# Performance work log

Measured on AMD Instinct MI355X. Metric: run time of the kernel, lower is better.

## Reference

```python
import jax, jax.numpy as jnp
import numpy as np

B, S, I, H, O = 256, 512, 128, 256, 1


def setup_inputs() -> dict:
    key = jax.random.key(0)
    ks = jax.random.split(key, 12)
    s_a = 1.0 / np.sqrt(H + I)
    s_g = 1.0 / np.sqrt(H)
    s_f = 1.0 / np.sqrt(H)
    return {
        "x": jax.random.normal(ks[0], (B, S, I), dtype=jnp.float32),
        # input attention linear: (H+I) -> I
        "W_a": jax.random.uniform(ks[1], (I, H + I), minval=-s_a, maxval=s_a),
        "b_a": jax.random.uniform(ks[2], (I,), minval=-s_a, maxval=s_a),
        # GRUCell params (torch layout: [3H, I] / [3H, H], gate order r,z,n)
        "W_ih": jax.random.uniform(ks[3], (3 * H, I), minval=-s_g, maxval=s_g),
        "b_ih": jax.random.uniform(ks[4], (3 * H,), minval=-s_g, maxval=s_g),
        "W_hh": jax.random.uniform(ks[5], (3 * H, H), minval=-s_g, maxval=s_g),
        "b_hh": jax.random.uniform(ks[6], (3 * H,), minval=-s_g, maxval=s_g),
        # temporal attention linear: H -> 1
        "W_t": jax.random.uniform(ks[7], (1, H), minval=-s_f, maxval=s_f),
        "b_t": jax.random.uniform(ks[8], (1,), minval=-s_f, maxval=s_f),
        # output fc: H -> O
        "W_f": jax.random.uniform(ks[9], (O, H), minval=-s_f, maxval=s_f),
        "b_f": jax.random.uniform(ks[10], (O,), minval=-s_f, maxval=s_f),
    }


def reference(x, W_a, b_a, W_ih, b_ih, W_hh, b_hh, W_t, b_t, W_f, b_f):
    def step(h, x_t):  # h: [B,H], x_t: [B,I]
        combined = jnp.concatenate([x_t, h], axis=1)            # [B, I+H]
        scores = jnp.tanh(combined @ W_a.T + b_a)               # [B, I]
        alpha = jax.nn.softmax(scores, axis=1)                  # [B, I]
        xw = alpha * x_t                                        # [B, I]
        gi = xw @ W_ih.T + b_ih                                 # [B, 3H]
        gh = h @ W_hh.T + b_hh                                  # [B, 3H]
        i_r, i_z, i_n = jnp.split(gi, 3, axis=1)
        h_r, h_z, h_n = jnp.split(gh, 3, axis=1)
        r = jax.nn.sigmoid(i_r + h_r)
        z = jax.nn.sigmoid(i_z + h_z)
        n = jnp.tanh(i_n + r * h_n)
        h_new = (1.0 - z) * n + z * h
        return h_new, h_new

    h0 = jnp.zeros((x.shape[0], W_hh.shape[1]), dtype=x.dtype)
    xs = jnp.transpose(x, (1, 0, 2))                            # [S,B,I]
    _, hs = jax.lax.scan(step, h0, xs)                          # hs: [S,B,H]
    enc = jnp.transpose(hs, (1, 0, 2))                          # [B,S,H]

    t_scores = jnp.tanh(enc @ W_t.T + b_t)                      # [B,S,1]
    beta = jax.nn.softmax(t_scores, axis=1)                     # softmax over time
    context = jnp.sum(beta * enc, axis=1)                       # [B,H]
    logits = context @ W_f.T + b_f                              # [B,O]
    return jax.nn.sigmoid(logits)
```

## Files before the change

### kernel.cpp

```cpp
#include <hip/hip_runtime.h>
#include <math.h>

#define BB 256
#define SS 512
#define II 128
#define HH 256

typedef unsigned short ushort_t;
typedef unsigned int uint32;

#define OFF_WA   0
#define OFF_BA   49152
#define OFF_WIH  49280
#define OFF_BIH  147584
#define OFF_WHH  148352
#define OFF_BHH  344960
#define OFF_WT   345728
#define OFF_BT   345984
#define OFF_WF   345992
#define OFF_BF   346248
#define OFF_WAH  346256
#define OFF_GIX  379024

#define WHH_LC   12

__device__ __forceinline__ float b2f(ushort_t u) {
    union { uint32 i; float f; } v; v.i = ((uint32)u) << 16; return v.f;
}
__device__ __forceinline__ float lo2f(uint32 w) {
    union { uint32 i; float f; } v; v.i = w << 16; return v.f;
}
__device__ __forceinline__ float hi2f(uint32 w) {
    union { uint32 i; float f; } v; v.i = w & 0xFFFF0000u; return v.f;
}
__device__ __forceinline__ ushort_t f2b(float f) {
    union { float f; uint32 i; } v; v.f = f;
    uint32 r = (v.i + 0x7FFFu + ((v.i >> 16) & 1u)) >> 16;
    return (ushort_t)r;
}
__device__ __forceinline__ uint32 pack2(float a, float b) {
    return (uint32)f2b(a) | ((uint32)f2b(b) << 16);
}

#if __has_builtin(__builtin_amdgcn_fdot2_f32_bf16)
typedef __bf16 v2bf __attribute__((ext_vector_type(2)));
__device__ __forceinline__ float dot2u(uint32 w, uint32 v, float acc) {
    return __builtin_amdgcn_fdot2_f32_bf16(
        __builtin_bit_cast(v2bf, w), __builtin_bit_cast(v2bf, v), acc, false);
}
#else
__device__ __forceinline__ float dot2u(uint32 w, uint32 v, float acc) {
    acc = fmaf(lo2f(w), lo2f(v), acc);
    return fmaf(hi2f(w), hi2f(v), acc);
}
#endif
__device__ __forceinline__ float dot4(uint4 w, uint4 v, float acc) {
    acc = dot2u(w.x, v.x, acc); acc = dot2u(w.y, v.y, acc);
    acc = dot2u(w.z, v.z, acc); return dot2u(w.w, v.w, acc);
}

__global__ void cvt_f32_bf16(const float* __restrict__ src, ushort_t* __restrict__ dst, int n) {
    int i = blockIdx.x * 256 + threadIdx.x;
    if (i < n) dst[i] = f2b(src[i]);
}

__global__ void cvt_swz(const float* __restrict__ src, ushort_t* __restrict__ dst,
                        int rows, int chunks, int srcStride, int colOff) {
    int t = blockIdx.x * 256 + threadIdx.x;
    if (t >= rows * chunks) return;
    int row = t / chunks, c = t % chunks;
    const float* s = src + (size_t)row * srcStride + colOff + c * 8;
    uint4 v;
    v.x = pack2(s[0], s[1]); v.y = pack2(s[2], s[3]);
    v.z = pack2(s[4], s[5]); v.w = pack2(s[6], s[7]);
    ((uint4*)dst)[((size_t)(row >> 6) * chunks + c) * 64 + (row & 63)] = v;
}

__global__ __launch_bounds__(512, 2) void gix_kernel(
    const float* __restrict__ x, const ushort_t* __restrict__ wsb,
    float* __restrict__ gix)
{
    const int b = blockIdx.x, tid = threadIdx.x;
    const int r4 = tid >> 7, i = tid & 127;
    __shared__ __align__(16) uint32 sxp[4][64];

    uint4 w[16];
    const uint4* wa_g = (const uint4*)(wsb + OFF_WA);
    const size_t gb = (size_t)(i >> 6) * 48 * 64 + (i & 63);
    #pragma unroll
    for (int c = 0; c < 16; ++c) w[c] = wa_g[gb + (size_t)c * 64];

    const float* xb = x + (size_t)b * SS * II;
    float* gout = gix + (size_t)b * SS * II;
    for (int j = 0; j < SS; j += 4) {
        float v = xb[(j + r4) * II + i];
        float vn = __shfl_down(v, 1);
        if (!(i & 1)) sxp[r4][i >> 1] = pack2(v, vn);
        __syncthreads();
        const uint4* sx4 = (const uint4*)sxp[r4];
        float acc = 0.f;
        #pragma unroll
        for (int c = 0; c < 16; ++c) acc = dot4(w[c], sx4[c], acc);
        gout[(j + r4) * II + i] = acc;
        __syncthreads();
    }
}

template <int GIX>
__global__ __launch_bounds__(1024, 4) void da_rnn_kernel(
    const float* __restrict__ x,
    const ushort_t* __restrict__ wsb,
    const float* __restrict__ gix,
    float* __restrict__ out)
{
    const int b    = blockIdx.x;
    const int tid  = threadIdx.x;
    const int lane = tid & 63;
    const int wv   = tid >> 6;
    const bool is_gate = (tid < 3 * HH);

    __shared__ __align__(16) uint32 whh_lds[WHH_LC * 768 * 4];
    __shared__ __align__(16) uint32 s_xh_p[192];
    __shared__ __align__(16) uint32 sxw_p[64];
    __shared__ __align__(16) float  sred[256];
    __shared__ __align__(16) float  sgi[3 * HH];
    __shared__ __align__(16) float  sgh[3 * HH];
    __shared__ __align__(16) float  sx[2][II];
    __shared__ __align__(16) float  sgix[2][II];
    __shared__ float swave[4];
    __shared__ int   flag_red;
    __shared__ int   flag_xw;

    if (tid == 0) { flag_red = 0; flag_xw = 0; }
    if (tid < II) s_xh_p[64 + tid] = 0u;

    uint4 wreg[16];
    const int a   = tid - 3 * HH;
    const int row = a & 127;
    const int s   = a >> 7;
    const uint4* whh_base = (const uint4*)(wsb + OFF_WHH) + (size_t)wv * 32 * 64 + lane;
    const uint4* wa_st = nullptr;
    float bias_i = 0.f, bias_h = 0.f, ba_a = 0.f, ba_b = 0.f;

    if (is_gate) {
        const uint4* wih_g = (const uint4*)(wsb + OFF_WIH) + (size_t)wv * 16 * 64 + lane;
        #pragma unroll
        for (int c = 0; c < 16; ++c) wreg[c] = wih_g[c * 64];
        bias_i = b2f(wsb[OFF_BIH + tid]);
        bias_h = b2f(wsb[OFF_BHH + tid]);
        #pragma unroll
        for (int c = 0; c < WHH_LC; ++c)
            ((uint4*)whh_lds)[(wv * WHH_LC + c) * 64 + lane] = whh_base[c * 64];
    } else {
        if (GIX) {
            const uint4* wah_g = (const uint4*)(wsb + OFF_WAH);
            const size_t gbh = ((size_t)(row >> 6) * 32 + s * 16) * 64 + (row & 63);
            #pragma unroll
            for (int i = 0; i < 16; ++i) wreg[i] = wah_g[gbh + (size_t)i * 64];
        } else {
            const uint4* wa_g = (const uint4*)(wsb + OFF_WA);
            const size_t gbase = ((size_t)(row >> 6) * 48 + s * 24) * 64 + (row & 63);
            #pragma unroll
            for (int i = 0; i < 16; ++i) wreg[i] = wa_g[gbase + (size_t)i * 64];
            wa_st = wa_g + gbase + (size_t)16 * 64;
        }
        ba_a = b2f(wsb[OFF_BA + lane]);
        ba_b = b2f(wsb[OFF_BA + 64 + lane]);
    }

    float h_reg = 0.f, c_reg = 0.f, m_run = -2.0f, l_run = 0.f;
    float wt_j = 0.f, wf_j = 0.f, bt_r = 0.f;
    if (tid < HH) {
        wt_j = b2f(wsb[OFF_WT + tid]);
        wf_j = b2f(wsb[OFF_WF + tid]);
        bt_r = b2f(wsb[OFF_BT]);
    }

    const float* xrow  = x + (size_t)b * SS * II;
    const float* grow0 = GIX ? (gix + (size_t)b * SS * II) : nullptr;
    if (!is_gate && a >= 64 && a < 192) {
        const int idx = a - 64;
        float v = xrow[idx];
        sx[0][idx] = v;
        if (!GIX) {
            float vn = __shfl_down(v, 1);
            if (!(idx & 1)) s_xh_p[idx >> 1] = pack2(v, vn);
        }
    }
    if (GIX && !is_gate && a >= 192) {
        const int l = a - 192;
        sgix[0][l]      = grow0[l];
        sgix[0][64 + l] = grow0[64 + l];
    }
    __syncthreads();

    const uint4* st4 = (const uint4*)s_xh_p;
    const uint4* shp = (const uint4*)s_xh_p + 16;
    const uint4* xwp = (const uint4*)sxw_p;
    const uint4* whl = (const uint4*)whh_lds + (size_t)(wv * WHH_LC) * 64 + lane;

    for (int t = 0; t < SS; ++t) {
        const int p = t & 1;

        if (is_gate) {
            float gh = bias_h;
            #pragma unroll
            for (int c = 0; c < WHH_LC; ++c) gh = dot4(whl[c * 64], shp[c], gh);
            #pragma unroll 4
            for (int c = WHH_LC; c < 32; ++c) gh = dot4(whh_base[c * 64], shp[c], gh);
            sgh[tid] = gh;
            while (__hip_atomic_load(&flag_xw, __ATOMIC_ACQUIRE,
                                     __HIP_MEMORY_SCOPE_WORKGROUP) <= t) {}
            float gi = bias_i;
            #pragma unroll
            for (int c = 0; c < 16; ++c) gi = dot4(wreg[c], xwp[c], gi);
            sgi[tid] = gi;
        } else {
            float acc = 0.f;
            if (GIX) {
                #pragma unroll
                for (int i = 0; i < 16; ++i) acc = dot4(wreg[i], shp[s * 16 + i], acc);
            } else {
                #pragma unroll
                for (int i = 0; i < 16; ++i) acc = dot4(wreg[i], st4[s * 24 + i], acc);
                #pragma unroll 4
                for (int i = 0; i < 8; ++i) acc = dot4(wa_st[i * 64], st4[s * 24 + 16 + i], acc);
            }
            sred[a] = acc;
            if (lane == 0)
                __hip_atomic_fetch_add(&flag_red, 1, __ATOMIC_ACQ_REL,
                                       __HIP_MEMORY_SCOPE_WORKGROUP);
            const int tgt = 4 * (t + 1);
            while (__hip_atomic_load(&flag_red, __ATOMIC_ACQUIRE,
                                     __HIP_MEMORY_SCOPE_WORKGROUP) < tgt) {}
            if (a < 64) {
                float s_a = sred[lane] + sred[128 + lane] + ba_a;
                float s_b = sred[64 + lane] + sred[192 + lane] + ba_b;
                if (GIX) { s_a += sgix[p][lane]; s_b += sgix[p][64 + lane]; }
                s_a = tanhf(s_a); s_b = tanhf(s_b);
                float m = fmaxf(s_a, s_b);
                for (int off = 32; off; off >>= 1) m = fmaxf(m, __shfl_xor(m, off));
                float e_a = expf(s_a - m), e_b = expf(s_b - m);
                float sum = e_a + e_b;
                for (int off = 32; off; off >>= 1) sum += __shfl_xor(sum, off);
                float inv = 1.f / sum;
                float xa = e_a * inv * sx[p][lane];
                float xb = e_b * inv * sx[p][64 + lane];
                float xa1 = __shfl_down(xa, 1), xb1 = __shfl_down(xb, 1);
                if (!(lane & 1)) {
                    sxw_p[lane >> 1]        = pack2(xa, xa1);
                    sxw_p[32 + (lane >> 1)] = pack2(xb, xb1);
                }
                if (lane == 0)
                    __hip_atomic_store(&flag_xw, t + 1, __ATOMIC_RELEASE,
                                       __HIP_MEMORY_SCOPE_WORKGROUP);
            } else if (a >= 64 && a < 192 && t + 1 < SS) {
                const int idx = a - 64;
                float v = xrow[(t + 1) * II + idx];
                sx[p ^ 1][idx] = v;
                if (!GIX) {
                    float vn = __shfl_down(v, 1);
                    if (!(idx & 1)) s_xh_p[idx >> 1] = pack2(v, vn);
                }
            } else if (GIX && a >= 192 && t + 1 < SS) {
                const float* gr = grow0 + (size_t)(t + 1) * II;
                const int l = a - 192;
                sgix[p ^ 1][l]      = gr[l];
                sgix[p ^ 1][64 + l] = gr[64 + l];
            }
        }
        __syncthreads();

        if (tid < HH) {
            const float r = 1.f / (1.f + expf(-(sgi[tid] + sgh[tid])));
            const float z = 1.f / (1.f + expf(-(sgi[tid + HH] + sgh[tid + HH])));
            const float n = tanhf(sgi[tid + 2 * HH] + r * sgh[tid + 2 * HH]);
            h_reg = (1.f - z) * n + z * h_reg;
            float hn2 = __shfl_down(h_reg, 1);
            if (!(tid & 1)) s_xh_p[64 + (tid >> 1)] = pack2(h_reg, hn2);
            float pd = wt_j * h_reg;
            for (int off = 32; off; off >>= 1) pd += __shfl_down(pd, off);
            if (lane == 0) swave[wv] = pd;
        }
        __syncthreads();

        if (tid < HH) {
            float dot = swave[0] + swave[1] + swave[2] + swave[3] + bt_r;
            float st = tanhf(dot);
            float mn = fmaxf(m_run, st);
            float aa = expf(m_run - mn), ww = expf(st - mn);
            l_run = l_run * aa + ww;
            m_run = mn;
            c_reg = c_reg * aa + ww * h_reg;
        }
    }

    __syncthreads();
    if (tid < HH) {
        float ctx = c_reg / l_run;
        float pd = wf_j * ctx;
        for (int off = 32; off; off >>= 1) pd += __shfl_down(pd, off);
        if (lane == 0) swave[wv] = pd;
    }
    __syncthreads();
    if (tid == 0) {
        float logit = swave[0] + swave[1] + swave[2] + swave[3] + b2f(wsb[OFF_BF]);
        out[b] = 1.f / (1.f + expf(-logit));
    }
}

extern "C" void kernel_launch(void* const* d_in, const int* in_sizes, int n_in,
                              void* d_out, int out_size, void* d_ws, size_t ws_size,
                              hipStream_t stream) {
    ushort_t* wsb = (ushort_t*)d_ws;
    const size_t WS_NEED = (size_t)OFF_GIX * 2 + (size_t)BB * SS * II * 4;
    const bool use_gix = ws_size >= WS_NEED;

    cvt_swz<<<dim3((128 * 48 + 255) / 256), dim3(256), 0, stream>>>(
        (const float*)d_in[1], wsb + OFF_WA, 128, 48, 384, 0);
    cvt_swz<<<dim3((768 * 16 + 255) / 256), dim3(256), 0, stream>>>(
        (const float*)d_in[3], wsb + OFF_WIH, 768, 16, 128, 0);
    cvt_swz<<<dim3((768 * 32 + 255) / 256), dim3(256), 0, stream>>>(
        (const float*)d_in[5], wsb + OFF_WHH, 768, 32, 256, 0);
    if (use_gix)
        cvt_swz<<<dim3((128 * 32 + 255) / 256), dim3(256), 0, stream>>>(
            (const float*)d_in[1], wsb + OFF_WAH, 128, 32, 384, 128);

    struct { int src_idx; int off; int n; } cv[7] = {
        {2, OFF_BA,  II}, {4, OFF_BIH, 3 * HH}, {6, OFF_BHH, 3 * HH},
        {7, OFF_WT,  HH}, {8, OFF_BT, 1}, {9, OFF_WF, HH}, {10, OFF_BF, 1},
    };
    for (int i = 0; i < 7; ++i) {
        int blocks = (cv[i].n + 255) / 256;
        cvt_f32_bf16<<<dim3(blocks), dim3(256), 0, stream>>>(
            (const float*)d_in[cv[i].src_idx], wsb + cv[i].off, cv[i].n);
    }

    float* gixf = (float*)(wsb + OFF_GIX);
    if (use_gix) {
        gix_kernel<<<dim3(BB), dim3(512), 0, stream>>>(
            (const float*)d_in[0], wsb, gixf);
        da_rnn_kernel<1><<<dim3(BB), dim3(1024), 0, stream>>>(
            (const float*)d_in[0], wsb, gixf, (float*)d_out);
    } else {
        da_rnn_kernel<0><<<dim3(BB), dim3(1024), 0, stream>>>(
            (const float*)d_in[0], wsb, nullptr, (float*)d_out);
    }
}
```

Baseline: 2.396 ms.

## Break dot-product dependency chains and software-prefetch global W_hh chunks in GRU loop

The gate-thread W_hh and W_ih dot products, and the GIX attention reduction, are split into four independent accumulators to shorten FMA dependency chains. The global-memory part of W_hh is software-pipelined: the next batch of four uint4 chunks is loaded while the current batch is consumed, and the first batch is prefetched before the next step's barrier wait. Gate waves also raise their scheduling priority with s_setprio around the compute sections. This aims to hide global-load latency on the serial recurrent critical path, at the cost of more registers, which may lower occupancy.

```diff
diff --git a/kernel.cpp b/kernel.cpp
--- a/kernel.cpp
+++ b/kernel.cpp
@@ -23,6 +23,7 @@
 #define OFF_GIX  379024
 
 #define WHH_LC   12
+#define NBATCH   ((32 - WHH_LC) / 4)
 
 __device__ __forceinline__ float b2f(ushort_t u) {
     union { uint32 i; float f; } v; v.i = ((uint32)u) << 16; return v.f;
@@ -192,6 +193,12 @@
         sgix[0][l]      = grow0[l];
         sgix[0][64 + l] = grow0[64 + l];
     }
+
+    uint4 p0 = {}, p1 = {}, p2 = {}, p3 = {};
+    if (is_gate) {
+        const uint4* nb = whh_base + WHH_LC * 64;
+        p0 = nb[0]; p1 = nb[64]; p2 = nb[128]; p3 = nb[192];
+    }
     __syncthreads();
 
     const uint4* st4 = (const uint4*)s_xh_p;
@@ -203,24 +210,62 @@
         const int p = t & 1;
 
         if (is_gate) {
-            float gh = bias_h;
-            #pragma unroll
-            for (int c = 0; c < WHH_LC; ++c) gh = dot4(whl[c * 64], shp[c], gh);
-            #pragma unroll 4
-            for (int c = WHH_LC; c < 32; ++c) gh = dot4(whh_base[c * 64], shp[c], gh);
-            sgh[tid] = gh;
+            __builtin_amdgcn_s_setprio(1);
+            float g0 = bias_h, g1 = 0.f, g2 = 0.f, g3 = 0.f;
+            #pragma unroll
+            for (int c = 0; c < WHH_LC; c += 4) {
+                g0 = dot4(whl[(c + 0) * 64], shp[c + 0], g0);
+                g1 = dot4(whl[(c + 1) * 64], shp[c + 1], g1);
+                g2 = dot4(whl[(c + 2) * 64], shp[c + 2], g2);
+                g3 = dot4(whl[(c + 3) * 64], shp[c + 3], g3);
+            }
+            #pragma unroll
+            for (int bb = 0; bb < NBATCH; ++bb) {
+                uint4 n0, n1, n2, n3;
+                if (bb + 1 < NBATCH) {
+                    const uint4* nb = whh_base + (WHH_LC + 4 * (bb + 1)) * 64;
+                    n0 = nb[0]; n1 = nb[64]; n2 = nb[128]; n3 = nb[192];
+                }
+                const int c = WHH_LC + 4 * bb;
+                g0 = dot4(p0, shp[c + 0], g0);
+                g1 = dot4(p1, shp[c + 1], g1);
+                g2 = dot4(p2, shp[c + 2], g2);
+                g3 = dot4(p3, shp[c + 3], g3);
+                if (bb + 1 < NBATCH) { p0 = n0; p1 = n1; p2 = n2; p3 = n3; }
+            }
+            sgh[tid] = (g0 + g1) + (g2 + g3);
+            __builtin_amdgcn_s_setprio(0);
             while (__hip_atomic_load(&flag_xw, __ATOMIC_ACQUIRE,
                                      __HIP_MEMORY_SCOPE_WORKGROUP) <= t) {}
-            float gi = bias_i;
-            #pragma unroll
-            for (int c = 0; c < 16; ++c) gi = dot4(wreg[c], xwp[c], gi);
-            sgi[tid] = gi;
+            __builtin_amdgcn_s_setprio(1);
+            float q0 = bias_i, q1 = 0.f, q2 = 0.f, q3 = 0.f;
+            #pragma unroll
+            for (int c = 0; c < 16; c += 4) {
+                q0 = dot4(wreg[c + 0], xwp[c + 0], q0);
+                q1 = dot4(wreg[c + 1], xwp[c + 1], q1);
+                q2 = dot4(wreg[c + 2], xwp[c + 2], q2);
+                q3 = dot4(wreg[c + 3], xwp[c + 3], q3);
+            }
+            sgi[tid] = (q0 + q1) + (q2 + q3);
+            {
+                const uint4* nb = whh_base + WHH_LC * 64;
+                p0 = nb[0]; p1 = nb[64]; p2 = nb[128]; p3 = nb[192];
+            }
+            __builtin_amdgcn_s_setprio(0);
         } else {
-            float acc = 0.f;
+            float acc;
             if (GIX) {
+                float a0 = 0.f, a1 = 0.f, a2 = 0.f, a3 = 0.f;
                 #pragma unroll
-                for (int i = 0; i < 16; ++i) acc = dot4(wreg[i], shp[s * 16 + i], acc);
+                for (int i = 0; i < 16; i += 4) {
+                    a0 = dot4(wreg[i + 0], shp[s * 16 + i + 0], a0);
+                    a1 = dot4(wreg[i + 1], shp[s * 16 + i + 1], a1);
+                    a2 = dot4(wreg[i + 2], shp[s * 16 + i + 2], a2);
+                    a3 = dot4(wreg[i + 3], shp[s * 16 + i + 3], a3);
+                }
+                acc = (a0 + a1) + (a2 + a3);
             } else {
+                acc = 0.f;
                 #pragma unroll
                 for (int i = 0; i < 16; ++i) acc = dot4(wreg[i], st4[s * 24 + i], acc);
                 #pragma unroll 4
```

Result: slower. 4.559 ms (+90.3%).

## Stream W_hh chunks through an LDS ring via async global-to-LDS DMA

Applied to the files above, without the earlier changes.

Cuts the LDS-resident share of W_hh from 12 to 8 chunks. The remaining chunks are streamed through a per-wave 4-slot LDS ring filled with global_load_lds, so each global fetch overlaps the dot products on earlier chunks. The recurrent dot products are split across several independent accumulators to shorten the FMA dependency chains. The two __syncthreads are replaced by a bare s_barrier that waits only on lgkmcnt, leaving the outstanding DMA loads in flight across barriers. This relies on hand-placed waitcnt counts and wrap-around indexing being correct, and adds LDS pressure from the ring buffer.

```diff
diff --git a/kernel.cpp b/kernel.cpp
--- a/kernel.cpp
+++ b/kernel.cpp
@@ -22,7 +22,10 @@
 #define OFF_WAH  346256
 #define OFF_GIX  379024
 
-#define WHH_LC   12
+#define WHH_LC   8
+#define NSLOT    4
+#define NSTREAM  (32 - WHH_LC)
+#define WRAP_IT  (NSTREAM - NSLOT - 1)
 
 __device__ __forceinline__ float b2f(ushort_t u) {
     union { uint32 i; float f; } v; v.i = ((uint32)u) << 16; return v.f;
@@ -57,6 +60,18 @@
 __device__ __forceinline__ float dot4(uint4 w, uint4 v, float acc) {
     acc = dot2u(w.x, v.x, acc); acc = dot2u(w.y, v.y, acc);
     acc = dot2u(w.z, v.z, acc); return dot2u(w.w, v.w, acc);
+}
+
+__device__ __forceinline__ void lds_dma16(const uint4* g, uint4* l) {
+    __builtin_amdgcn_global_load_lds(
+        (const __attribute__((address_space(1))) void*)g,
+        (__attribute__((address_space(3))) void*)l, 16, 0, 0);
+}
+
+__device__ __forceinline__ void barrier_soft() {
+    asm volatile("s_waitcnt lgkmcnt(0)" ::: "memory");
+    __builtin_amdgcn_s_barrier();
+    asm volatile("" ::: "memory");
 }
 
 __global__ void cvt_f32_bf16(const float* __restrict__ src, ushort_t* __restrict__ dst, int n) {
@@ -120,6 +135,7 @@
     const bool is_gate = (tid < 3 * HH);
 
     __shared__ __align__(16) uint32 whh_lds[WHH_LC * 768 * 4];
+    __shared__ __align__(16) uint32 ring_lds[12 * NSLOT * 256];
     __shared__ __align__(16) uint32 s_xh_p[192];
     __shared__ __align__(16) uint32 sxw_p[64];
     __shared__ __align__(16) float  sred[256];
@@ -194,6 +210,16 @@
     }
     __syncthreads();
 
+    uint4* const ring4 = (uint4*)ring_lds;
+    const int ring_idx = wv * NSLOT * 64;
+    const uint4* nxt = whh_base + (WHH_LC + NSLOT) * 64;
+
+    if (is_gate) {
+        #pragma unroll
+        for (int s2 = 0; s2 < NSLOT; ++s2)
+            lds_dma16(whh_base + (WHH_LC + s2) * 64, ring4 + ring_idx + s2 * 64);
+    }
+
     const uint4* st4 = (const uint4*)s_xh_p;
     const uint4* shp = (const uint4*)s_xh_p + 16;
     const uint4* xwp = (const uint4*)sxw_p;
@@ -203,12 +229,30 @@
         const int p = t & 1;
 
         if (is_gate) {
-            float gh = bias_h;
-            #pragma unroll
-            for (int c = 0; c < WHH_LC; ++c) gh = dot4(whl[c * 64], shp[c], gh);
-            #pragma unroll 4
-            for (int c = WHH_LC; c < 32; ++c) gh = dot4(whh_base[c * 64], shp[c], gh);
-            sgh[tid] = gh;
+            float g0 = bias_h, g1 = 0.f, g2 = 0.f, g3 = 0.f;
+            #pragma unroll
+            for (int c = 0; c < WHH_LC; c += 4) {
+                g0 = dot4(whl[(c + 0) * 64], shp[c + 0], g0);
+                g1 = dot4(whl[(c + 1) * 64], shp[c + 1], g1);
+                g2 = dot4(whl[(c + 2) * 64], shp[c + 2], g2);
+                g3 = dot4(whl[(c + 3) * 64], shp[c + 3], g3);
+            }
+            #pragma unroll
+            for (int i = 0; i < NSTREAM; ++i) {
+                const int sl = i & 3;
+                asm volatile("s_waitcnt vmcnt(3)" ::: "memory");
+                uint4 w = ring4[ring_idx + sl * 64 + lane];
+                asm volatile("s_waitcnt lgkmcnt(0)" ::: "memory");
+                __builtin_amdgcn_sched_barrier(0);
+                lds_dma16(nxt, ring4 + ring_idx + sl * 64);
+                nxt += 64;
+                if (i == WRAP_IT) nxt = whh_base + WHH_LC * 64;
+                if      (sl == 0) g0 = dot4(w, shp[WHH_LC + i], g0);
+                else if (sl == 1) g1 = dot4(w, shp[WHH_LC + i], g1);
+                else if (sl == 2) g2 = dot4(w, shp[WHH_LC + i], g2);
+                else              g3 = dot4(w, shp[WHH_LC + i], g3);
+            }
+            sgh[tid] = (g0 + g1) + (g2 + g3);
             while (__hip_atomic_load(&flag_xw, __ATOMIC_ACQUIRE,
                                      __HIP_MEMORY_SCOPE_WORKGROUP) <= t) {}
             float gi = bias_i;
@@ -216,11 +260,17 @@
             for (int c = 0; c < 16; ++c) gi = dot4(wreg[c], xwp[c], gi);
             sgi[tid] = gi;
         } else {
-            float acc = 0.f;
+            float acc;
             if (GIX) {
+                float a0 = 0.f, a1 = 0.f;
                 #pragma unroll
-                for (int i = 0; i < 16; ++i) acc = dot4(wreg[i], shp[s * 16 + i], acc);
+                for (int i = 0; i < 16; i += 2) {
+                    a0 = dot4(wreg[i + 0], shp[s * 16 + i + 0], a0);
+                    a1 = dot4(wreg[i + 1], shp[s * 16 + i + 1], a1);
+                }
+                acc = a0 + a1;
             } else {
+                acc = 0.f;
                 #pragma unroll
                 for (int i = 0; i < 16; ++i) acc = dot4(wreg[i], st4[s * 24 + i], acc);
                 #pragma unroll 4
@@ -269,7 +319,7 @@
                 sgix[p ^ 1][64 + l] = gr[64 + l];
             }
         }
-        __syncthreads();
+        barrier_soft();
 
         if (tid < HH) {
             const float r = 1.f / (1.f + expf(-(sgi[tid] + sgh[tid])));
@@ -282,7 +332,7 @@
             for (int off = 32; off; off >>= 1) pd += __shfl_down(pd, off);
             if (lane == 0) swave[wv] = pd;
         }
-        __syncthreads();
+        barrier_soft();
 
         if (tid < HH) {
             float dot = swave[0] + swave[1] + swave[2] + swave[3] + bt_r;
```

After: 5.198 ms. 117% more time.
